# Kernel optimization log

Measured on AMD Instinct MI355X. Metric: run time of the kernel, lower is better.

## Reference

```python
import jax, jax.numpy as jnp
import numpy as np

B_SZ, L, D, N = 4, 2048, 768, 16


def setup_inputs() -> dict:
    key = jax.random.key(0)
    ks = jax.random.split(key, 8)
    x = jax.random.normal(ks[0], (B_SZ, L, D), dtype=jnp.float32)
    # A_log initialized as log(arange(1..N)) repeated over d, as in the module
    A_log = jnp.log(jnp.broadcast_to(jnp.arange(1, N + 1, dtype=jnp.float32), (D, N)))
    # s_b_c: Linear(D, 2N)
    W_bc = jax.random.normal(ks[1], (2 * N, D), dtype=jnp.float32) / jnp.sqrt(D)
    b_bc = jnp.zeros((2 * N,), dtype=jnp.float32)
    # s_1: Linear(D, 1)
    W_1 = jax.random.normal(ks[2], (1, D), dtype=jnp.float32) / jnp.sqrt(D)
    b_1 = jnp.zeros((1,), dtype=jnp.float32)
    # s_delta: Linear(1, D)
    W_d = jax.random.normal(ks[3], (D, 1), dtype=jnp.float32)
    b_d = jnp.zeros((D,), dtype=jnp.float32)
    return {"x": x, "A_log": A_log, "W_bc": W_bc, "b_bc": b_bc,
            "W_1": W_1, "b_1": b_1, "W_d": W_d, "b_d": b_d}


def reference(x, A_log, W_bc, b_bc, W_1, b_1, W_d, b_d):
    b, l, d = x.shape
    n = A_log.shape[1]
    A = -jnp.exp(A_log)                                   # (d, n)
    BandC = x @ W_bc.T + b_bc                             # (b, l, 2n)
    Bm, Cm = BandC[..., :n], BandC[..., n:]               # (b, l, n) each
    # delta = softplus(s_delta(s_1(x)))  -> (b, l, d)
    s1 = x @ W_1.T + b_1                                  # (b, l, 1)
    delta = jax.nn.softplus(s1 @ W_d.T + b_d)             # (b, l, d)
    deltaA = jnp.exp(jnp.einsum('bld,dn->bldn', delta, A))        # (b, l, d, n)
    deltaB_u = jnp.einsum('bld,bln,bld->bldn', delta, Bm, x)      # (b, l, d, n)

    # sequential selective-scan over time with lax.scan
    dA_t = jnp.moveaxis(deltaA, 1, 0)      # (l, b, d, n)
    dBu_t = jnp.moveaxis(deltaB_u, 1, 0)   # (l, b, d, n)
    C_t = jnp.moveaxis(Cm, 1, 0)           # (l, b, n)

    def step(h, inp):
        dA_i, dBu_i, c_i = inp
        h = dA_i * h + dBu_i               # (b, d, n)
        y = jnp.einsum('bdn,bn->bd', h, c_i)
        return h, y

    h0 = jnp.zeros((b, d, n), dtype=x.dtype)
    _, ys = jax.lax.scan(step, h0, (dA_t, dBu_t, C_t))
    return jnp.moveaxis(ys, 0, 1)          # (b, l, d)
```

## Files before the change

### kernel.cpp

```cpp
#include <hip/hip_runtime.h>

#define L_SEQ 2048
#define D_DIM 768
#define N_ST 16
#define NB 4
#define NJ 33
#define BCS 48
#define NROWS (NB * L_SEQ)
#define PROJ_ELEMS (NROWS * NJ)
#define DN (D_DIM * N_ST)

#define DSPLIT 8
#define DSEG (D_DIM / DSPLIT)
#define DK 32
#define NCHUNK (DSEG / DK)
#define RB 128
#define XST 132
#define WST 64

typedef float v2f __attribute__((ext_vector_type(2)));

__device__ __forceinline__ float fast_exp2(float x) {
#if __has_builtin(__builtin_amdgcn_exp2f)
  return __builtin_amdgcn_exp2f(x);
#else
  return __expf(x * 0.69314718055994531f);
#endif
}

__device__ __forceinline__ float softplus_f(float v) {
  float e = fast_exp2(v * 1.44269504088896f);
  float l = __log2f(1.0f + e) * 0.69314718055994531f;
  return (v > 15.0f) ? v : l;
}

__device__ __forceinline__ void pow_tree2(float e1, v2f pw2[8]) {
  float e2s = e1 * e1;
  float e4s = e2s * e2s;
  float e8s = e4s * e4s;
  v2f s2 = {e2s, e2s}, s4 = {e4s, e4s}, s8 = {e8s, e8s};
  pw2[0] = (v2f){e1, e2s};
  pw2[1] = pw2[0] * s2;
  pw2[2] = pw2[0] * s4;
  pw2[3] = pw2[1] * s4;
  pw2[4] = pw2[0] * s8;
  pw2[5] = pw2[1] * s8;
  pw2[6] = pw2[2] * s8;
  pw2[7] = pw2[3] * s8;
}

__global__ __launch_bounds__(256) void k_proj_gemm(
    const float* __restrict__ x, const float* __restrict__ W_bc,
    const float* __restrict__ W_1, float* __restrict__ PBC) {
  __shared__ float xs_t[DK * XST];
  __shared__ float ws_t[DK * WST];

  const int ds  = blockIdx.x % DSPLIT;
  const int rb0 = (blockIdx.x / DSPLIT) * RB;
  const int dbase = ds * DSEG;
  const int tid = threadIdx.x;
  const int rg = tid & 31;
  const int jg = tid >> 5;

  float acc[4][5];
#pragma unroll
  for (int i = 0; i < 4; ++i)
#pragma unroll
    for (int k = 0; k < 5; ++k) acc[i][k] = 0.0f;

  const int lrow = tid >> 1;
  const int lhalf = (tid & 1) * 16;
  const float* xg_row = x + (size_t)(rb0 + lrow) * D_DIM + dbase + lhalf;

  for (int ch = 0; ch < NCHUNK; ++ch) {
    const int dc = dbase + ch * DK;
    float4 xv[4];
#pragma unroll
    for (int q = 0; q < 4; ++q)
      xv[q] = *(const float4*)(xg_row + ch * DK + q * 4);
    float wv[8];
    int widx[8];
#pragma unroll
    for (int u = 0; u < 8; ++u) {
      int idx = tid + u * 256;
      int dk = idx >> 6, slot = idx & 63;
      int wjg = slot >> 3, wk = slot & 7;
      int j = wjg + 8 * wk;
      float v = 0.0f;
      if (wk < 5) {
        if (j < 32)       v = W_bc[(size_t)j * D_DIM + dc + dk];
        else if (j == 32) v = W_1[dc + dk];
      }
      wv[u] = v; widx[u] = dk * WST + slot;
    }
    __syncthreads();
#pragma unroll
    for (int q = 0; q < 4; ++q) {
      xs_t[(lhalf + q * 4 + 0) * XST + lrow] = xv[q].x;
      xs_t[(lhalf + q * 4 + 1) * XST + lrow] = xv[q].y;
      xs_t[(lhalf + q * 4 + 2) * XST + lrow] = xv[q].z;
      xs_t[(lhalf + q * 4 + 3) * XST + lrow] = xv[q].w;
    }
#pragma unroll
    for (int u = 0; u < 8; ++u) ws_t[widx[u]] = wv[u];
    __syncthreads();
#pragma unroll 8
    for (int dk = 0; dk < DK; ++dk) {
      float4 xr = *(const float4*)&xs_t[dk * XST + rg * 4];
      float4 wr = *(const float4*)&ws_t[dk * WST + jg * 8];
      float w4  = ws_t[dk * WST + jg * 8 + 4];
      float xa[4] = {xr.x, xr.y, xr.z, xr.w};
      float wa[5] = {wr.x, wr.y, wr.z, wr.w, w4};
#pragma unroll
      for (int i = 0; i < 4; ++i)
#pragma unroll
        for (int k = 0; k < 5; ++k)
          acc[i][k] = fmaf(xa[i], wa[k], acc[i][k]);
    }
  }

  float* pb = PBC + (size_t)ds * PROJ_ELEMS;
#pragma unroll
  for (int i = 0; i < 4; ++i) {
    int row = rb0 + rg * 4 + i;
#pragma unroll
    for (int k = 0; k < 5; ++k) {
      int j = jg + 8 * k;
      if (k < 4 || jg == 0) pb[(size_t)row * NJ + j] = acc[i][k];
    }
  }
}

__global__ __launch_bounds__(256) void k_proj_reduce(
    const float* __restrict__ PBC, const float* __restrict__ b_bc,
    const float* __restrict__ b_1, float* __restrict__ BC48) {
  const int idx = blockIdx.x * 256 + threadIdx.x;
  const int row = idx / NJ;
  const int j = idx - row * NJ;
  float s = 0.0f;
#pragma unroll
  for (int k = 0; k < DSPLIT; ++k) s += PBC[(size_t)k * PROJ_ELEMS + idx];
  s += (j < 32) ? b_bc[j] : b_1[0];
  BC48[(size_t)row * BCS + j] = s;
}

template <int LC>
__global__ __launch_bounds__(256) void k_scan1(
    const float* __restrict__ x, const float* __restrict__ A_log,
    const float* __restrict__ W_d, const float* __restrict__ b_d,
    const float* __restrict__ BC48, float* __restrict__ DS,
    float* __restrict__ H, int NC) {
  const int cb = blockIdx.x % 3;
  const int c  = (blockIdx.x / 3) % NC;
  const int b  = blockIdx.x / (3 * NC);
  const int d  = cb * 256 + threadIdx.x;

  const float wd = W_d[d], bd = b_d[d];
  float Aln[N_ST];
  {
    const float4* al4 = (const float4*)(A_log + (size_t)d * N_ST);
#pragma unroll
    for (int q = 0; q < 4; ++q) {
      float4 v = al4[q];
      Aln[4*q+0] = -__expf(v.x) * 1.44269504088896f;
      Aln[4*q+1] = -__expf(v.y) * 1.44269504088896f;
      Aln[4*q+2] = -__expf(v.z) * 1.44269504088896f;
      Aln[4*q+3] = -__expf(v.w) * 1.44269504088896f;
    }
  }
  bool geom = true;
#pragma unroll
  for (int n = 1; n < N_ST; ++n) {
    float ref = (float)(n + 1) * Aln[0];
    geom = geom && (fabsf(Aln[n] - ref) <= 1e-4f * fabsf(ref) + 1e-12f);
  }
  const float a0 = Aln[0];

  v2f h2[8];
#pragma unroll
  for (int k = 0; k < 8; ++k) h2[k] = (v2f){0.0f, 0.0f};
  float dsum = 0.0f;

  const int l0 = c * LC;
  const float* bc = BC48 + (size_t)(b * L_SEQ + l0) * BCS;
  const float* xp = x + (size_t)(b * L_SEQ + l0) * D_DIM + d;

  if (geom) {
#pragma unroll 8
    for (int l = 0; l < LC; ++l) {
      const float* r = bc + l * BCS;
      float4 B0 = *(const float4*)(r + 0);
      float4 B1 = *(const float4*)(r + 4);
      float4 B2 = *(const float4*)(r + 8);
      float4 B3 = *(const float4*)(r + 12);
      float s1 = r[32];
      float delta = softplus_f(fmaf(s1, wd, bd));
      float xv = xp[(size_t)l * D_DIM];
      float f = delta * xv;
      dsum += delta;
      v2f pw2[8];
      pow_tree2(fast_exp2(a0 * delta), pw2);
      v2f f2 = {f, f};
      h2[0] = pw2[0] * h2[0] + f2 * (v2f){B0.x, B0.y};
      h2[1] = pw2[1] * h2[1] + f2 * (v2f){B0.z, B0.w};
      h2[2] = pw2[2] * h2[2] + f2 * (v2f){B1.x, B1.y};
      h2[3] = pw2[3] * h2[3] + f2 * (v2f){B1.z, B1.w};
      h2[4] = pw2[4] * h2[4] + f2 * (v2f){B2.x, B2.y};
      h2[5] = pw2[5] * h2[5] + f2 * (v2f){B2.z, B2.w};
      h2[6] = pw2[6] * h2[6] + f2 * (v2f){B3.x, B3.y};
      h2[7] = pw2[7] * h2[7] + f2 * (v2f){B3.z, B3.w};
    }
  } else {
#pragma unroll 4
    for (int l = 0; l < LC; ++l) {
      const float* r = bc + l * BCS;
      float s1 = r[32];
      float delta = softplus_f(fmaf(s1, wd, bd));
      float f = delta * xp[(size_t)l * D_DIM];
      dsum += delta;
#pragma unroll
      for (int k = 0; k < 8; ++k) {
        h2[k].x = fmaf(fast_exp2(delta * Aln[2*k]),   h2[k].x, f * r[2*k]);
        h2[k].y = fmaf(fast_exp2(delta * Aln[2*k+1]), h2[k].y, f * r[2*k+1]);
      }
    }
  }

  DS[((size_t)b * NC + c) * D_DIM + d] = dsum;
  size_t base = ((size_t)(b * NC + c) * D_DIM + d) * N_ST;
  float4* H4 = (float4*)(H + base);
#pragma unroll
  for (int q = 0; q < 4; ++q)
    H4[q] = make_float4(h2[2*q].x, h2[2*q].y, h2[2*q+1].x, h2[2*q+1].y);
}

__global__ __launch_bounds__(256) void k_combine(
    const float* __restrict__ A_log, const float* __restrict__ DS,
    float* __restrict__ H, int NC) {
  const int b  = blockIdx.x / 48;
  const int tl = (blockIdx.x % 48) * 256 + threadIdx.x;
  const int d = tl >> 4, n = tl & 15;
  const float Aln1 = -__expf(A_log[d * N_ST + n]) * 1.44269504088896f;
  const float* dsp = DS + (size_t)b * NC * D_DIM + d;
  float* Hp = H + (size_t)b * NC * DN + tl;

  float h = 0.0f;
  float pds[8], ph[8];
#pragma unroll
  for (int k = 0; k < 8; ++k) {
    pds[k] = dsp[(size_t)k * D_DIM];
    ph[k]  = Hp[(size_t)k * DN];
  }
  for (int g = 0; g < NC; g += 8) {
    float nds[8], nh[8];
    if (g + 8 < NC) {
#pragma unroll
      for (int k = 0; k < 8; ++k) {
        nds[k] = dsp[(size_t)(g + 8 + k) * D_DIM];
        nh[k]  = Hp[(size_t)(g + 8 + k) * DN];
      }
    }
#pragma unroll
    for (int k = 0; k < 8; ++k) {
      float p = fast_exp2(Aln1 * pds[k]);
      Hp[(size_t)(g + k) * DN] = h;
      h = fmaf(p, h, ph[k]);
    }
#pragma unroll
    for (int k = 0; k < 8; ++k) { pds[k] = nds[k]; ph[k] = nh[k]; }
  }
}

template <int LC>
__global__ __launch_bounds__(256) void k_scan2(
    const float* __restrict__ x, const float* __restrict__ A_log,
    const float* __restrict__ W_d, const float* __restrict__ b_d,
    const float* __restrict__ BC48, const float* __restrict__ HIN,
    float* __restrict__ out, int NC) {
  const int cb = blockIdx.x % 3;
  const int c  = (blockIdx.x / 3) % NC;
  const int b  = blockIdx.x / (3 * NC);
  const int d  = cb * 256 + threadIdx.x;

  const float wd = W_d[d], bd = b_d[d];
  float Aln[N_ST];
  {
    const float4* al4 = (const float4*)(A_log + (size_t)d * N_ST);
#pragma unroll
    for (int q = 0; q < 4; ++q) {
      float4 v = al4[q];
      Aln[4*q+0] = -__expf(v.x) * 1.44269504088896f;
      Aln[4*q+1] = -__expf(v.y) * 1.44269504088896f;
      Aln[4*q+2] = -__expf(v.z) * 1.44269504088896f;
      Aln[4*q+3] = -__expf(v.w) * 1.44269504088896f;
    }
  }
  bool geom = true;
#pragma unroll
  for (int n = 1; n < N_ST; ++n) {
    float ref = (float)(n + 1) * Aln[0];
    geom = geom && (fabsf(Aln[n] - ref) <= 1e-4f * fabsf(ref) + 1e-12f);
  }
  const float a0 = Aln[0];

  v2f h2[8];
  {
    size_t base = ((size_t)(b * NC + c) * D_DIM + d) * N_ST;
    const float4* HIN4 = (const float4*)(HIN + base);
#pragma unroll
    for (int q = 0; q < 4; ++q) {
      float4 v = HIN4[q];
      h2[2*q]   = (v2f){v.x, v.y};
      h2[2*q+1] = (v2f){v.z, v.w};
    }
  }

  const int l0 = c * LC;
  const float* bc = BC48 + (size_t)(b * L_SEQ + l0) * BCS;
  const float* xp = x + (size_t)(b * L_SEQ + l0) * D_DIM + d;
  float* op = out + (size_t)(b * L_SEQ + l0) * D_DIM + d;

  if (geom) {
#pragma unroll 8
    for (int l = 0; l < LC; ++l) {
      const float* r = bc + l * BCS;
      float4 B0 = *(const float4*)(r + 0);
      float4 B1 = *(const float4*)(r + 4);
      float4 B2 = *(const float4*)(r + 8);
      float4 B3 = *(const float4*)(r + 12);
      float4 C0 = *(const float4*)(r + 16);
      float4 C1 = *(const float4*)(r + 20);
      float4 C2 = *(const float4*)(r + 24);
      float4 C3 = *(const float4*)(r + 28);
      float s1 = r[32];
      float delta = softplus_f(fmaf(s1, wd, bd));
      float xv = xp[(size_t)l * D_DIM];
      float f = delta * xv;
      v2f pw2[8];
      pow_tree2(fast_exp2(a0 * delta), pw2);
      v2f f2 = {f, f};
      v2f y2 = {0.0f, 0.0f};
      h2[0] = pw2[0] * h2[0] + f2 * (v2f){B0.x, B0.y};  y2 += h2[0] * (v2f){C0.x, C0.y};
      h2[1] = pw2[1] * h2[1] + f2 * (v2f){B0.z, B0.w};  y2 += h2[1] * (v2f){C0.z, C0.w};
      h2[2] = pw2[2] * h2[2] + f2 * (v2f){B1.x, B1.y};  y2 += h2[2] * (v2f){C1.x, C1.y};
      h2[3] = pw2[3] * h2[3] + f2 * (v2f){B1.z, B1.w};  y2 += h2[3] * (v2f){C1.z, C1.w};
      h2[4] = pw2[4] * h2[4] + f2 * (v2f){B2.x, B2.y};  y2 += h2[4] * (v2f){C2.x, C2.y};
      h2[5] = pw2[5] * h2[5] + f2 * (v2f){B2.z, B2.w};  y2 += h2[5] * (v2f){C2.z, C2.w};
      h2[6] = pw2[6] * h2[6] + f2 * (v2f){B3.x, B3.y};  y2 += h2[6] * (v2f){C3.x, C3.y};
      h2[7] = pw2[7] * h2[7] + f2 * (v2f){B3.z, B3.w};  y2 += h2[7] * (v2f){C3.z, C3.w};
      op[(size_t)l * D_DIM] = y2.x + y2.y;
    }
  } else {
#pragma unroll 4
    for (int l = 0; l < LC; ++l) {
      const float* r = bc + l * BCS;
      float s1 = r[32];
      float delta = softplus_f(fmaf(s1, wd, bd));
      float f = delta * xp[(size_t)l * D_DIM];
      float y = 0.0f;
#pragma unroll
      for (int k = 0; k < 8; ++k) {
        h2[k].x = fmaf(fast_exp2(delta * Aln[2*k]),   h2[k].x, f * r[2*k]);
        h2[k].y = fmaf(fast_exp2(delta * Aln[2*k+1]), h2[k].y, f * r[2*k+1]);
        y = fmaf(h2[k].x, r[16 + 2*k], y);
        y = fmaf(h2[k].y, r[16 + 2*k + 1], y);
      }
      op[(size_t)l * D_DIM] = y;
    }
  }
}

extern "C" void kernel_launch(void* const* d_in, const int* in_sizes, int n_in,
                              void* d_out, int out_size, void* d_ws, size_t ws_size,
                              hipStream_t stream) {
  const float* x     = (const float*)d_in[0];
  const float* A_log = (const float*)d_in[1];
  const float* W_bc  = (const float*)d_in[2];
  const float* b_bc  = (const float*)d_in[3];
  const float* W_1   = (const float*)d_in[4];
  const float* b_1   = (const float*)d_in[5];
  const float* W_d   = (const float*)d_in[6];
  const float* b_d   = (const float*)d_in[7];
  float* out = (float*)d_out;
  float* ws  = (float*)d_ws;

  int NC = 64;
  {
    size_t need = ((size_t)NROWS * BCS + 8ull * PROJ_ELEMS +
                   (3072ull + 49152ull) * 64) * 4ull;
    if (ws_size < need) NC = 32;
  }

  float* BC48 = ws;
  float* PBC  = ws + (size_t)NROWS * BCS;
  float* DSb  = PBC + (size_t)DSPLIT * PROJ_ELEMS;
  float* H    = DSb + (size_t)3072 * NC;

  k_proj_gemm<<<(NROWS / RB) * DSPLIT, 256, 0, stream>>>(x, W_bc, W_1, PBC);
  k_proj_reduce<<<(PROJ_ELEMS + 255) / 256, 256, 0, stream>>>(PBC, b_bc, b_1, BC48);

  const int gs = 3 * NB * NC;
  if (NC == 64) {
    k_scan1<32><<<gs, 256, 0, stream>>>(x, A_log, W_d, b_d, BC48, DSb, H, NC);
    k_combine<<<192, 256, 0, stream>>>(A_log, DSb, H, NC);
    k_scan2<32><<<gs, 256, 0, stream>>>(x, A_log, W_d, b_d, BC48, H, out, NC);
  } else {
    k_scan1<64><<<gs, 256, 0, stream>>>(x, A_log, W_d, b_d, BC48, DSb, H, NC);
    k_combine<<<192, 256, 0, stream>>>(A_log, DSb, H, NC);
    k_scan2<64><<<gs, 256, 0, stream>>>(x, A_log, W_d, b_d, BC48, H, out, NC);
  }
}
```

Before: 151.9 us.

## Emit local-state outputs in first scan pass and apply carry-in correction afterward

The first chunked scan pass now computes y from the zero-initialized local state and writes it to the output, while also saving chunk end-states and delta sums. The second pass no longer reruns the recurrence. It adds a correction term built from the carried-in state, decayed by the cumulative delta, times C, and it skips chunk 0. The projection split-K reduction kernel and its partial buffer are replaced by atomicAdd into a zeroed BC buffer, and the scan kernels get an occupancy hint. Costs include a read-modify-write of the output, a memset, atomic traffic, and non-deterministic summation order.

Result: slower. 217.7 us (+43.3%).

```diff
diff --git a/kernel.cpp b/kernel.cpp
--- a/kernel.cpp
+++ b/kernel.cpp
@@ -7,7 +7,6 @@
 #define NJ 33
 #define BCS 48
 #define NROWS (NB * L_SEQ)
-#define PROJ_ELEMS (NROWS * NJ)
 #define DN (D_DIM * N_ST)
 
 #define DSPLIT 8
@@ -51,7 +50,8 @@
 
 __global__ __launch_bounds__(256) void k_proj_gemm(
     const float* __restrict__ x, const float* __restrict__ W_bc,
-    const float* __restrict__ W_1, float* __restrict__ PBC) {
+    const float* __restrict__ W_1, const float* __restrict__ b_bc,
+    const float* __restrict__ b_1, float* __restrict__ BC48) {
   __shared__ float xs_t[DK * XST];
   __shared__ float ws_t[DK * WST];
 
@@ -119,37 +119,27 @@
     }
   }
 
-  float* pb = PBC + (size_t)ds * PROJ_ELEMS;
 #pragma unroll
   for (int i = 0; i < 4; ++i) {
     int row = rb0 + rg * 4 + i;
 #pragma unroll
     for (int k = 0; k < 5; ++k) {
       int j = jg + 8 * k;
-      if (k < 4 || jg == 0) pb[(size_t)row * NJ + j] = acc[i][k];
-    }
-  }
-}
-
-__global__ __launch_bounds__(256) void k_proj_reduce(
-    const float* __restrict__ PBC, const float* __restrict__ b_bc,
-    const float* __restrict__ b_1, float* __restrict__ BC48) {
-  const int idx = blockIdx.x * 256 + threadIdx.x;
-  const int row = idx / NJ;
-  const int j = idx - row * NJ;
-  float s = 0.0f;
-#pragma unroll
-  for (int k = 0; k < DSPLIT; ++k) s += PBC[(size_t)k * PROJ_ELEMS + idx];
-  s += (j < 32) ? b_bc[j] : b_1[0];
-  BC48[(size_t)row * BCS + j] = s;
+      if (k < 4 || jg == 0) {
+        float v = acc[i][k];
+        if (ds == 0) v += (j < 32) ? b_bc[j] : b_1[0];
+        atomicAdd(&BC48[(size_t)row * BCS + j], v);
+      }
+    }
+  }
 }
 
 template <int LC>
-__global__ __launch_bounds__(256) void k_scan1(
+__global__ __launch_bounds__(256, 6) void k_scan1(
     const float* __restrict__ x, const float* __restrict__ A_log,
     const float* __restrict__ W_d, const float* __restrict__ b_d,
     const float* __restrict__ BC48, float* __restrict__ DS,
-    float* __restrict__ H, int NC) {
+    float* __restrict__ H, float* __restrict__ out, int NC) {
   const int cb = blockIdx.x % 3;
   const int c  = (blockIdx.x / 3) % NC;
   const int b  = blockIdx.x / (3 * NC);
@@ -180,140 +170,6 @@
 #pragma unroll
   for (int k = 0; k < 8; ++k) h2[k] = (v2f){0.0f, 0.0f};
   float dsum = 0.0f;
-
-  const int l0 = c * LC;
-  const float* bc = BC48 + (size_t)(b * L_SEQ + l0) * BCS;
-  const float* xp = x + (size_t)(b * L_SEQ + l0) * D_DIM + d;
-
-  if (geom) {
-#pragma unroll 8
-    for (int l = 0; l < LC; ++l) {
-      const float* r = bc + l * BCS;
-      float4 B0 = *(const float4*)(r + 0);
-      float4 B1 = *(const float4*)(r + 4);
-      float4 B2 = *(const float4*)(r + 8);
-      float4 B3 = *(const float4*)(r + 12);
-      float s1 = r[32];
-      float delta = softplus_f(fmaf(s1, wd, bd));
-      float xv = xp[(size_t)l * D_DIM];
-      float f = delta * xv;
-      dsum += delta;
-      v2f pw2[8];
-      pow_tree2(fast_exp2(a0 * delta), pw2);
-      v2f f2 = {f, f};
-      h2[0] = pw2[0] * h2[0] + f2 * (v2f){B0.x, B0.y};
-      h2[1] = pw2[1] * h2[1] + f2 * (v2f){B0.z, B0.w};
-      h2[2] = pw2[2] * h2[2] + f2 * (v2f){B1.x, B1.y};
-      h2[3] = pw2[3] * h2[3] + f2 * (v2f){B1.z, B1.w};
-      h2[4] = pw2[4] * h2[4] + f2 * (v2f){B2.x, B2.y};
-      h2[5] = pw2[5] * h2[5] + f2 * (v2f){B2.z, B2.w};
-      h2[6] = pw2[6] * h2[6] + f2 * (v2f){B3.x, B3.y};
-      h2[7] = pw2[7] * h2[7] + f2 * (v2f){B3.z, B3.w};
-    }
-  } else {
-#pragma unroll 4
-    for (int l = 0; l < LC; ++l) {
-      const float* r = bc + l * BCS;
-      float s1 = r[32];
-      float delta = softplus_f(fmaf(s1, wd, bd));
-      float f = delta * xp[(size_t)l * D_DIM];
-      dsum += delta;
-#pragma unroll
-      for (int k = 0; k < 8; ++k) {
-        h2[k].x = fmaf(fast_exp2(delta * Aln[2*k]),   h2[k].x, f * r[2*k]);
-        h2[k].y = fmaf(fast_exp2(delta * Aln[2*k+1]), h2[k].y, f * r[2*k+1]);
-      }
-    }
-  }
-
-  DS[((size_t)b * NC + c) * D_DIM + d] = dsum;
-  size_t base = ((size_t)(b * NC + c) * D_DIM + d) * N_ST;
-  float4* H4 = (float4*)(H + base);
-#pragma unroll
-  for (int q = 0; q < 4; ++q)
-    H4[q] = make_float4(h2[2*q].x, h2[2*q].y, h2[2*q+1].x, h2[2*q+1].y);
-}
-
-__global__ __launch_bounds__(256) void k_combine(
-    const float* __restrict__ A_log, const float* __restrict__ DS,
-    float* __restrict__ H, int NC) {
-  const int b  = blockIdx.x / 48;
-  const int tl = (blockIdx.x % 48) * 256 + threadIdx.x;
-  const int d = tl >> 4, n = tl & 15;
-  const float Aln1 = -__expf(A_log[d * N_ST + n]) * 1.44269504088896f;
-  const float* dsp = DS + (size_t)b * NC * D_DIM + d;
-  float* Hp = H + (size_t)b * NC * DN + tl;
-
-  float h = 0.0f;
-  float pds[8], ph[8];
-#pragma unroll
-  for (int k = 0; k < 8; ++k) {
-    pds[k] = dsp[(size_t)k * D_DIM];
-    ph[k]  = Hp[(size_t)k * DN];
-  }
-  for (int g = 0; g < NC; g += 8) {
-    float nds[8], nh[8];
-    if (g + 8 < NC) {
-#pragma unroll
-      for (int k = 0; k < 8; ++k) {
-        nds[k] = dsp[(size_t)(g + 8 + k) * D_DIM];
-        nh[k]  = Hp[(size_t)(g + 8 + k) * DN];
-      }
-    }
-#pragma unroll
-    for (int k = 0; k < 8; ++k) {
-      float p = fast_exp2(Aln1 * pds[k]);
-      Hp[(size_t)(g + k) * DN] = h;
-      h = fmaf(p, h, ph[k]);
-    }
-#pragma unroll
-    for (int k = 0; k < 8; ++k) { pds[k] = nds[k]; ph[k] = nh[k]; }
-  }
-}
-
-template <int LC>
-__global__ __launch_bounds__(256) void k_scan2(
-    const float* __restrict__ x, const float* __restrict__ A_log,
-    const float* __restrict__ W_d, const float* __restrict__ b_d,
-    const float* __restrict__ BC48, const float* __restrict__ HIN,
-    float* __restrict__ out, int NC) {
-  const int cb = blockIdx.x % 3;
-  const int c  = (blockIdx.x / 3) % NC;
-  const int b  = blockIdx.x / (3 * NC);
-  const int d  = cb * 256 + threadIdx.x;
-
-  const float wd = W_d[d], bd = b_d[d];
-  float Aln[N_ST];
-  {
-    const float4* al4 = (const float4*)(A_log + (size_t)d * N_ST);
-#pragma unroll
-    for (int q = 0; q < 4; ++q) {
-      float4 v = al4[q];
-      Aln[4*q+0] = -__expf(v.x) * 1.44269504088896f;
-      Aln[4*q+1] = -__expf(v.y) * 1.44269504088896f;
-      Aln[4*q+2] = -__expf(v.z) * 1.44269504088896f;
-      Aln[4*q+3] = -__expf(v.w) * 1.44269504088896f;
-    }
-  }
-  bool geom = true;
-#pragma unroll
-  for (int n = 1; n < N_ST; ++n) {
-    float ref = (float)(n + 1) * Aln[0];
-    geom = geom && (fabsf(Aln[n] - ref) <= 1e-4f * fabsf(ref) + 1e-12f);
-  }
-  const float a0 = Aln[0];
-
-  v2f h2[8];
-  {
-    size_t base = ((size_t)(b * NC + c) * D_DIM + d) * N_ST;
-    const float4* HIN4 = (const float4*)(HIN + base);
-#pragma unroll
-    for (int q = 0; q < 4; ++q) {
-      float4 v = HIN4[q];
-      h2[2*q]   = (v2f){v.x, v.y};
-      h2[2*q+1] = (v2f){v.z, v.w};
-    }
-  }
 
   const int l0 = c * LC;
   const float* bc = BC48 + (size_t)(b * L_SEQ + l0) * BCS;
@@ -336,6 +192,7 @@
       float delta = softplus_f(fmaf(s1, wd, bd));
       float xv = xp[(size_t)l * D_DIM];
       float f = delta * xv;
+      dsum += delta;
       v2f pw2[8];
       pow_tree2(fast_exp2(a0 * delta), pw2);
       v2f f2 = {f, f};
@@ -357,6 +214,7 @@
       float s1 = r[32];
       float delta = softplus_f(fmaf(s1, wd, bd));
       float f = delta * xp[(size_t)l * D_DIM];
+      dsum += delta;
       float y = 0.0f;
 #pragma unroll
       for (int k = 0; k < 8; ++k) {
@@ -366,6 +224,144 @@
         y = fmaf(h2[k].y, r[16 + 2*k + 1], y);
       }
       op[(size_t)l * D_DIM] = y;
+    }
+  }
+
+  DS[((size_t)b * NC + c) * D_DIM + d] = dsum;
+  size_t base = ((size_t)(b * NC + c) * D_DIM + d) * N_ST;
+  float4* H4 = (float4*)(H + base);
+#pragma unroll
+  for (int q = 0; q < 4; ++q)
+    H4[q] = make_float4(h2[2*q].x, h2[2*q].y, h2[2*q+1].x, h2[2*q+1].y);
+}
+
+__global__ __launch_bounds__(256) void k_combine(
+    const float* __restrict__ A_log, const float* __restrict__ DS,
+    float* __restrict__ H, int NC) {
+  const int b  = blockIdx.x / 48;
+  const int tl = (blockIdx.x % 48) * 256 + threadIdx.x;
+  const int d = tl >> 4, n = tl & 15;
+  const float Aln1 = -__expf(A_log[d * N_ST + n]) * 1.44269504088896f;
+  const float* dsp = DS + (size_t)b * NC * D_DIM + d;
+  float* Hp = H + (size_t)b * NC * DN + tl;
+
+  float h = 0.0f;
+  float pds[8], ph[8];
+#pragma unroll
+  for (int k = 0; k < 8; ++k) {
+    pds[k] = dsp[(size_t)k * D_DIM];
+    ph[k]  = Hp[(size_t)k * DN];
+  }
+  for (int g = 0; g < NC; g += 8) {
+    float nds[8], nh[8];
+    if (g + 8 < NC) {
+#pragma unroll
+      for (int k = 0; k < 8; ++k) {
+        nds[k] = dsp[(size_t)(g + 8 + k) * D_DIM];
+        nh[k]  = Hp[(size_t)(g + 8 + k) * DN];
+      }
+    }
+#pragma unroll
+    for (int k = 0; k < 8; ++k) {
+      float p = fast_exp2(Aln1 * pds[k]);
+      Hp[(size_t)(g + k) * DN] = h;
+      h = fmaf(p, h, ph[k]);
+    }
+#pragma unroll
+    for (int k = 0; k < 8; ++k) { pds[k] = nds[k]; ph[k] = nh[k]; }
+  }
+}
+
+template <int LC>
+__global__ __launch_bounds__(256, 6) void k_scan2(
+    const float* __restrict__ A_log, const float* __restrict__ W_d,
+    const float* __restrict__ b_d, const float* __restrict__ BC48,
+    const float* __restrict__ HIN, float* __restrict__ out, int NC) {
+  const int cb  = blockIdx.x % 3;
+  const int idx = blockIdx.x / 3;
+  const int c   = idx % (NC - 1) + 1;
+  const int b   = idx / (NC - 1);
+  const int d   = cb * 256 + threadIdx.x;
+
+  const float wd = W_d[d], bd = b_d[d];
+  float Aln[N_ST];
+  {
+    const float4* al4 = (const float4*)(A_log + (size_t)d * N_ST);
+#pragma unroll
+    for (int q = 0; q < 4; ++q) {
+      float4 v = al4[q];
+      Aln[4*q+0] = -__expf(v.x) * 1.44269504088896f;
+      Aln[4*q+1] = -__expf(v.y) * 1.44269504088896f;
+      Aln[4*q+2] = -__expf(v.z) * 1.44269504088896f;
+      Aln[4*q+3] = -__expf(v.w) * 1.44269504088896f;
+    }
+  }
+  bool geom = true;
+#pragma unroll
+  for (int n = 1; n < N_ST; ++n) {
+    float ref = (float)(n + 1) * Aln[0];
+    geom = geom && (fabsf(Aln[n] - ref) <= 1e-4f * fabsf(ref) + 1e-12f);
+  }
+  const float a0 = Aln[0];
+
+  v2f hin2[8];
+  {
+    size_t base = ((size_t)(b * NC + c) * D_DIM + d) * N_ST;
+    const float4* HIN4 = (const float4*)(HIN + base);
+#pragma unroll
+    for (int q = 0; q < 4; ++q) {
+      float4 v = HIN4[q];
+      hin2[2*q]   = (v2f){v.x, v.y};
+      hin2[2*q+1] = (v2f){v.z, v.w};
+    }
+  }
+
+  const int l0 = c * LC;
+  const float* bc = BC48 + (size_t)(b * L_SEQ + l0) * BCS;
+  float* op = out + (size_t)(b * L_SEQ + l0) * D_DIM + d;
+
+  if (geom) {
+    float S = 0.0f;
+#pragma unroll 8
+    for (int l = 0; l < LC; ++l) {
+      const float* r = bc + l * BCS;
+      float yl = op[(size_t)l * D_DIM];
+      float4 C0 = *(const float4*)(r + 16);
+      float4 C1 = *(const float4*)(r + 20);
+      float4 C2 = *(const float4*)(r + 24);
+      float4 C3 = *(const float4*)(r + 28);
+      float s1 = r[32];
+      float delta = softplus_f(fmaf(s1, wd, bd));
+      S += delta;
+      v2f pw2[8];
+      pow_tree2(fast_exp2(a0 * S), pw2);
+      v2f acc = {0.0f, 0.0f};
+      acc += pw2[0] * (hin2[0] * (v2f){C0.x, C0.y});
+      acc += pw2[1] * (hin2[1] * (v2f){C0.z, C0.w});
+      acc += pw2[2] * (hin2[2] * (v2f){C1.x, C1.y});
+      acc += pw2[3] * (hin2[3] * (v2f){C1.z, C1.w});
+      acc += pw2[4] * (hin2[4] * (v2f){C2.x, C2.y});
+      acc += pw2[5] * (hin2[5] * (v2f){C2.z, C2.w});
+      acc += pw2[6] * (hin2[6] * (v2f){C3.x, C3.y});
+      acc += pw2[7] * (hin2[7] * (v2f){C3.z, C3.w});
+      op[(size_t)l * D_DIM] = yl + acc.x + acc.y;
+    }
+  } else {
+    float S = 0.0f;
+#pragma unroll 4
+    for (int l = 0; l < LC; ++l) {
+      const float* r = bc + l * BCS;
+      float yl = op[(size_t)l * D_DIM];
+      float s1 = r[32];
+      float delta = softplus_f(fmaf(s1, wd, bd));
+      S += delta;
+      float corr = 0.0f;
+#pragma unroll
+      for (int k = 0; k < 8; ++k) {
+        corr = fmaf(fast_exp2(Aln[2*k]   * S) * hin2[k].x, r[16 + 2*k],     corr);
+        corr = fmaf(fast_exp2(Aln[2*k+1] * S) * hin2[k].y, r[16 + 2*k + 1], corr);
+      }
+      op[(size_t)l * D_DIM] = yl + corr;
     }
   }
 }
@@ -386,27 +382,27 @@
 
   int NC = 64;
   {
-    size_t need = ((size_t)NROWS * BCS + 8ull * PROJ_ELEMS +
-                   (3072ull + 49152ull) * 64) * 4ull;
+    size_t need = ((size_t)NROWS * BCS + (3072ull + 49152ull) * 64) * 4ull;
     if (ws_size < need) NC = 32;
   }
 
   float* BC48 = ws;
-  float* PBC  = ws + (size_t)NROWS * BCS;
-  float* DSb  = PBC + (size_t)DSPLIT * PROJ_ELEMS;
+  float* DSb  = ws + (size_t)NROWS * BCS;
   float* H    = DSb + (size_t)3072 * NC;
 
-  k_proj_gemm<<<(NROWS / RB) * DSPLIT, 256, 0, stream>>>(x, W_bc, W_1, PBC);
-  k_proj_reduce<<<(PROJ_ELEMS + 255) / 256, 256, 0, stream>>>(PBC, b_bc, b_1, BC48);
-
-  const int gs = 3 * NB * NC;
+  hipMemsetAsync(BC48, 0, (size_t)NROWS * BCS * sizeof(float), stream);
+  k_proj_gemm<<<(NROWS / RB) * DSPLIT, 256, 0, stream>>>(
+      x, W_bc, W_1, b_bc, b_1, BC48);
+
+  const int gs1 = 3 * NB * NC;
+  const int gs2 = 3 * NB * (NC - 1);
   if (NC == 64) {
-    k_scan1<32><<<gs, 256, 0, stream>>>(x, A_log, W_d, b_d, BC48, DSb, H, NC);
+    k_scan1<32><<<gs1, 256, 0, stream>>>(x, A_log, W_d, b_d, BC48, DSb, H, out, NC);
     k_combine<<<192, 256, 0, stream>>>(A_log, DSb, H, NC);
-    k_scan2<32><<<gs, 256, 0, stream>>>(x, A_log, W_d, b_d, BC48, H, out, NC);
+    k_scan2<32><<<gs2, 256, 0, stream>>>(A_log, W_d, b_d, BC48, H, out, NC);
   } else {
-    k_scan1<64><<<gs, 256, 0, stream>>>(x, A_log, W_d, b_d, BC48, DSb, H, NC);
+    k_scan1<64><<<gs1, 256, 0, stream>>>(x, A_log, W_d, b_d, BC48, DSb, H, out, NC);
     k_combine<<<192, 256, 0, stream>>>(A_log, DSb, H, NC);
-    k_scan2<64><<<gs, 256, 0, stream>>>(x, A_log, W_d, b_d, BC48, H, out, NC);
-  }
-}
+    k_scan2<64><<<gs2, 256, 0, stream>>>(A_log, W_d, b_d, BC48, H, out, NC);
+  }
+}
```
